# Kernel tuning notes

Measured on AMD Instinct MI355X. Metric: run time of the kernel, lower is better.

The kernel has to match this reference:

```python
import jax, jax.numpy as jnp
import numpy as np

CODEBOOK_SIZE = 2048
LATENT_DIM = 256
COMMITMENT_BETA = 0.25
B, C, T = 16, LATENT_DIM, 2048


def setup_inputs() -> dict:
    key = jax.random.key(0)
    k1, k2 = jax.random.split(key)
    x = jax.random.normal(k1, (B, C, T), dtype=jnp.float32)
    # matches nn.Embedding.weight.data.uniform_(-1/K, 1/K)
    codebook = jax.random.uniform(
        k2, (CODEBOOK_SIZE, LATENT_DIM), dtype=jnp.float32,
        minval=-1.0 / CODEBOOK_SIZE, maxval=1.0 / CODEBOOK_SIZE)
    return {"x": x, "codebook": codebook}


def reference(x, codebook):
    b, c, t = x.shape
    # (B, C, T) -> (B*T, C)
    xf = jnp.transpose(x, (0, 2, 1)).reshape(b * t, c)
    # squared Euclidean distances; argmin is invariant to the sqrt in torch.cdist(p=2)
    x_sq = jnp.sum(xf * xf, axis=1, keepdims=True)            # (BT, 1)
    e_sq = jnp.sum(codebook * codebook, axis=1)[None, :]      # (1, K)
    d2 = x_sq - 2.0 * (xf @ codebook.T) + e_sq                # (BT, K)
    idx = jnp.argmin(d2, axis=-1)                             # (BT,)
    # gather codebook vectors -> (B, C, T)
    quant = codebook[idx].reshape(b, t, c).transpose(0, 2, 1)
    commitment_loss = COMMITMENT_BETA * jnp.mean(
        (jax.lax.stop_gradient(quant) - x) ** 2)
    codebook_loss = jnp.mean((quant - jax.lax.stop_gradient(x)) ** 2)
    # straight-through estimator
    quant_out = x + jax.lax.stop_gradient(quant - x)
    return quant_out, codebook_loss, commitment_loss, idx.reshape(b, t)
```

## Files before the change

kernel.cpp:

```cpp
#include <hip/hip_runtime.h>
#include <hip/hip_bf16.h>

#define KCODES 2048
#define DIM 256
#define TLEN 2048
#define NB 16
#define NROWS (NB * TLEN)
#define NELEM (NB * DIM * TLEN)
#define LOSS_OFF NELEM
#define IDX_OFF (NELEM + 2)

#define AMARGIN 1.8e-3f

#define CCAP 48

#define OFF_XSQ   0ull
#define OFF_ESQ   131072ull
#define OFF_KEYS  139264ull
#define OFF_BSUM  401408ull
#define OFF_EHI   532480ull
#define OFF_XHI   1581056ull
#define OFF_AMAX  18358272ull
#define OFF_MASK  22552576ull
#define WS_NEED   30941184ull

typedef __bf16 bf16x8 __attribute__((ext_vector_type(8)));
typedef float  f32x4  __attribute__((ext_vector_type(4)));

__device__ __forceinline__ float sq_rn(float v) { return __fmul_rn(v, v); }

__device__ __forceinline__ unsigned encf(float f) {
    unsigned u = __float_as_uint(f);
    return (u & 0x80000000u) ? ~u : (u | 0x80000000u);
}
__device__ __forceinline__ float decf(unsigned k) {
    return __uint_as_float((k & 0x80000000u) ? (k & 0x7FFFFFFFu) : ~k);
}

__global__ __launch_bounds__(256) void xsq_kernel(const float* __restrict__ x,
                                                  float* __restrict__ xsq) {
    int m = blockIdx.x * 256 + threadIdx.x;
    int b = m >> 11, t = m & (TLEN - 1);
    const float* p = x + (size_t)b * DIM * TLEN + t;
    float h[2];
#pragma unroll
    for (int half = 0; half < 2; ++half) {
        int c0 = half * 128;
        float r[8];
#pragma unroll
        for (int j = 0; j < 8; ++j) r[j] = sq_rn(p[(size_t)(c0 + j) * TLEN]);
        for (int i = 8; i < 128; i += 8) {
#pragma unroll
            for (int j = 0; j < 8; ++j)
                r[j] = __fadd_rn(r[j], sq_rn(p[(size_t)(c0 + i + j) * TLEN]));
        }
        h[half] = __fadd_rn(__fadd_rn(__fadd_rn(r[0], r[1]), __fadd_rn(r[2], r[3])),
                            __fadd_rn(__fadd_rn(r[4], r[5]), __fadd_rn(r[6], r[7])));
    }
    xsq[m] = __fadd_rn(h[0], h[1]);
}

__global__ __launch_bounds__(256) void esq_kernel(const float* __restrict__ cb,
                                                  float* __restrict__ esq) {
    int k = blockIdx.x * 256 + threadIdx.x;
    const float* p = cb + (size_t)k * DIM;
    float h[2];
#pragma unroll
    for (int half = 0; half < 2; ++half) {
        int c0 = half * 128;
        float r[8];
#pragma unroll
        for (int j = 0; j < 8; ++j) r[j] = sq_rn(p[c0 + j]);
        for (int i = 8; i < 128; i += 8) {
#pragma unroll
            for (int j = 0; j < 8; ++j)
                r[j] = __fadd_rn(r[j], sq_rn(p[c0 + i + j]));
        }
        h[half] = __fadd_rn(__fadd_rn(__fadd_rn(r[0], r[1]), __fadd_rn(r[2], r[3])),
                            __fadd_rn(__fadd_rn(r[4], r[5]), __fadd_rn(r[6], r[7])));
    }
    esq[k] = __fadd_rn(h[0], h[1]);
}

__global__ __launch_bounds__(256) void split_x_kernel(const float* __restrict__ x,
                                                      __hip_bfloat16* __restrict__ Xhi) {
    __shared__ float tb[32][72];
    int blk = blockIdx.x;
    int tt = blk & 31, cc = (blk >> 5) & 7, b = blk >> 8;
    int c0 = cc << 5, t0 = tt << 6;
    int tid = threadIdx.x;
    {
        int c_l = tid >> 3, t8 = (tid & 7) << 3;
        const float* src = x + (size_t)b * DIM * TLEN + (size_t)(c0 + c_l) * TLEN + t0 + t8;
        float4 v0 = *reinterpret_cast<const float4*>(src);
        float4 v1 = *reinterpret_cast<const float4*>(src + 4);
        tb[c_l][t8 + 0] = v0.x; tb[c_l][t8 + 1] = v0.y; tb[c_l][t8 + 2] = v0.z; tb[c_l][t8 + 3] = v0.w;
        tb[c_l][t8 + 4] = v1.x; tb[c_l][t8 + 5] = v1.y; tb[c_l][t8 + 6] = v1.z; tb[c_l][t8 + 7] = v1.w;
    }
    __syncthreads();
    {
        int cp = tid & 3, m_l = tid >> 2;
        size_t m = (size_t)b * TLEN + t0 + m_l;
        alignas(16) __hip_bfloat16 h8[8];
#pragma unroll
        for (int j = 0; j < 8; ++j)
            h8[j] = __float2bfloat16(tb[(cp << 3) + j][m_l]);
        *reinterpret_cast<int4*>(Xhi + m * DIM + c0 + (cp << 3)) = *reinterpret_cast<int4*>(h8);
    }
}

__global__ __launch_bounds__(256) void prep_e_kernel(const float* __restrict__ cb,
                                                     __hip_bfloat16* __restrict__ Ehi,
                                                     float* __restrict__ esq) {
    int tid = threadIdx.x;
    int w = tid >> 6, lane = tid & 63;
    int k = (blockIdx.x << 2) + w;
    const float* p = cb + (size_t)k * DIM;

    float4 v = *reinterpret_cast<const float4*>(p + (lane << 2));
    alignas(8) __hip_bfloat16 h4[4];
    h4[0] = __float2bfloat16(v.x); h4[1] = __float2bfloat16(v.y);
    h4[2] = __float2bfloat16(v.z); h4[3] = __float2bfloat16(v.w);
    *reinterpret_cast<int2*>(Ehi + (size_t)k * DIM + (lane << 2)) = *reinterpret_cast<int2*>(h4);

    if (lane < 16) {
        int c0 = (lane >> 3) << 7, j = lane & 7;
        float r = sq_rn(p[c0 + j]);
        for (int i = 8; i < 128; i += 8)
            r = __fadd_rn(r, sq_rn(p[c0 + i + j]));
        float a  = __fadd_rn(r,  __shfl_xor(r, 1, 16));
        float b2 = __fadd_rn(a,  __shfl_xor(a, 2, 16));
        float h  = __fadd_rn(b2, __shfl_xor(b2, 4, 16));
        float tot = __fadd_rn(h, __shfl_xor(h, 8, 16));
        if (lane == 0) esq[k] = tot;
    }
}

__global__ __launch_bounds__(256, 4) void mfma_dist_kernel(const __hip_bfloat16* __restrict__ Xhi,
                                                           const __hip_bfloat16* __restrict__ Ehi,
                                                           unsigned* __restrict__ amax_g,
                                                           unsigned long long* __restrict__ mask_g) {
    __shared__ __hip_bfloat16 Ah[128 * 64];
    __shared__ __hip_bfloat16 Bh[128 * 64];

    int blk = blockIdx.x;
    int nt = blk & 15, mt = blk >> 4;
    int m0 = mt << 7, n0 = nt << 7;
    int tid = threadIdx.x;
    int w = tid >> 6, lane = tid & 63;
    int q = lane >> 4, c = lane & 15;
    int mhalf = w >> 1, nhalf = w & 1;

    int srow = lane >> 3;
    int scol = ((lane & 7) ^ srow) << 3;
    const __hip_bfloat16* gA = Xhi + (size_t)(m0 + (w << 5) + srow) * DIM + scol;
    const __hip_bfloat16* gB = Ehi + (size_t)(n0 + (w << 5) + srow) * DIM + scol;

    f32x4 acc[4][4];
#pragma unroll
    for (int ci = 0; ci < 4; ++ci)
#pragma unroll
        for (int mi = 0; mi < 4; ++mi) acc[ci][mi] = (f32x4){0.f, 0.f, 0.f, 0.f};

    const char* AhB = reinterpret_cast<const char*>(Ah);
    const char* BhB = reinterpret_cast<const char*>(Bh);
    int swzc = (c & 7) << 4;

    for (int kk = 0; kk < DIM; kk += 64) {
#pragma unroll
        for (int j = 0; j < 4; ++j)
            __builtin_amdgcn_global_load_lds(
                (const __attribute__((address_space(1))) unsigned int*)(gA + (size_t)(j << 3) * DIM + kk),
                (__attribute__((address_space(3))) unsigned int*)(&Ah[((w << 2) + j) << 9]),
                16, 0, 0);
#pragma unroll
        for (int j = 0; j < 4; ++j)
            __builtin_amdgcn_global_load_lds(
                (const __attribute__((address_space(1))) unsigned int*)(gB + (size_t)(j << 3) * DIM + kk),
                (__attribute__((address_space(3))) unsigned int*)(&Bh[((w << 2) + j) << 9]),
                16, 0, 0);
        __syncthreads();
#pragma unroll
        for (int kh = 0; kh < 2; ++kh) {
            int swz = ((kh << 6) | (q << 4)) ^ swzc;
            bf16x8 xf[4], cf[4];
#pragma unroll
            for (int mi = 0; mi < 4; ++mi) {
                int row = (mhalf << 6) + (mi << 4) + c;
                xf[mi] = *reinterpret_cast<const bf16x8*>(AhB + (row << 7) + swz);
            }
#pragma unroll
            for (int ci = 0; ci < 4; ++ci) {
                int row = (nhalf << 6) + (ci << 4) + c;
                cf[ci] = *reinterpret_cast<const bf16x8*>(BhB + (row << 7) + swz);
            }
#pragma unroll
            for (int ci = 0; ci < 4; ++ci)
#pragma unroll
                for (int mi = 0; mi < 4; ++mi)
                    acc[ci][mi] = __builtin_amdgcn_mfma_f32_16x16x32_bf16(cf[ci], xf[mi], acc[ci][mi], 0, 0, 0);
        }
        __syncthreads();
    }

    int tb = (nt << 1) | nhalf;
#pragma unroll
    for (int mi = 0; mi < 4; ++mi) {
        float a16[16];
#pragma unroll
        for (int ci = 0; ci < 4; ++ci)
#pragma unroll
            for (int reg = 0; reg < 4; ++reg)
                a16[ci * 4 + reg] = acc[ci][mi][reg];
        float m01 = fmaxf(fmaxf(a16[0], a16[1]), fmaxf(a16[2], a16[3]));
        float m23 = fmaxf(fmaxf(a16[4], a16[5]), fmaxf(a16[6], a16[7]));
        float m45 = fmaxf(fmaxf(a16[8], a16[9]), fmaxf(a16[10], a16[11]));
        float m67 = fmaxf(fmaxf(a16[12], a16[13]), fmaxf(a16[14], a16[15]));
        float amax = fmaxf(fmaxf(m01, m23), fmaxf(m45, m67));
        amax = fmaxf(amax, __shfl_xor(amax, 16, 64));
        amax = fmaxf(amax, __shfl_xor(amax, 32, 64));
        float thrw = amax - AMARGIN;
        unsigned long long bits = 0;
#pragma unroll
        for (int v = 0; v < 16; ++v)
            if (a16[v] >= thrw)
                bits |= 1ULL << (((v >> 2) << 4) + (q << 2) + (v & 3));
        bits |= (unsigned long long)__shfl_xor((long long)bits, 16, 64);
        bits |= (unsigned long long)__shfl_xor((long long)bits, 32, 64);
        if (q == 0) {
            int m = m0 + (mhalf << 6) + (mi << 4) + c;
            amax_g[(size_t)tb * NROWS + m] = encf(amax);
            mask_g[(size_t)tb * NROWS + m] = bits;
        }
    }
}

__global__ __launch_bounds__(256) void recheck_kernel(const float* __restrict__ x,
                                                      const float* __restrict__ cb,
                                                      const float* __restrict__ esq,
                                                      const unsigned* __restrict__ amax_g,
                                                      const unsigned long long* __restrict__ mask_g,
                                                      unsigned long long* __restrict__ keys) {
    __shared__ float xT[DIM * 33];
    __shared__ int clist[32][CCAP];
    __shared__ int ccnt[32];

    int tid = threadIdx.x;
    int blk = blockIdx.x;
    int b = blk >> 6, t0 = (blk & 63) << 5;
    const float* xb = x + (size_t)b * DIM * TLEN + t0;

    if (tid < 32) ccnt[tid] = 0;
    {
        int tl = tid & 31, c8 = tid >> 5;
        for (int cc = 0; cc < 32; ++cc) {
            int c = (cc << 3) + c8;
            xT[c * 33 + tl] = xb[(size_t)c * TLEN + tl];
        }
    }
    __syncthreads();

    int g = tid >> 3, l3 = tid & 7;
    int m = (b << 11) + t0 + g;

    float h[2];
#pragma unroll
    for (int half = 0; half < 2; ++half) {
        int c0 = half * 128;
        float r = sq_rn(xT[(c0 + l3) * 33 + g]);
        for (int i = 8; i < 128; i += 8)
            r = __fadd_rn(r, sq_rn(xT[(c0 + i + l3) * 33 + g]));
        float a = __fadd_rn(r, __shfl_xor(r, 1, 8));
        float bb = __fadd_rn(a, __shfl_xor(a, 2, 8));
        h[half] = __fadd_rn(bb, __shfl_xor(bb, 4, 8));
    }
    float xs = __fadd_rn(h[0], h[1]);

    unsigned am4[4];
    unsigned ge = 0;
#pragma unroll
    for (int j = 0; j < 4; ++j) {
        am4[j] = amax_g[(size_t)(l3 * 4 + j) * NROWS + m];
        ge = max(ge, am4[j]);
    }
    for (int off = 1; off < 8; off <<= 1)
        ge = max(ge, (unsigned)__shfl_xor((int)ge, off, 8));
    float thr = decf(ge) - AMARGIN;

#pragma unroll
    for (int j = 0; j < 4; ++j) {
        if (decf(am4[j]) >= thr) {
            unsigned long long bits = mask_g[(size_t)(l3 * 4 + j) * NROWS + m];
            while (bits) {
                int p = __ffsll((long long)bits) - 1; bits &= bits - 1;
                int pos = atomicAdd(&ccnt[g], 1);
                if (pos < CCAP) clist[g][pos] = (l3 * 4 + j) * 64 + p;
            }
        }
    }
    __syncthreads();

    int cnt = ccnt[g];
    float bd = 3.4e38f; int bi = 0x7fffffff;

    if (cnt <= CCAP) {
        for (int j = l3; j < cnt; j += 8) {
            int n = clist[g][j];
            const float* crow = cb + (size_t)n * DIM;
            float d = 0.f;
            for (int k = 0; k < DIM; k += 4) {
                float4 cv = *reinterpret_cast<const float4*>(crow + k);
                d = fmaf(xT[(k + 0) * 33 + g], cv.x, d);
                d = fmaf(xT[(k + 1) * 33 + g], cv.y, d);
                d = fmaf(xT[(k + 2) * 33 + g], cv.z, d);
                d = fmaf(xT[(k + 3) * 33 + g], cv.w, d);
            }
            float d2 = __fadd_rn(__fadd_rn(xs, -2.0f * d), esq[n]);
            if (d2 < bd || (d2 == bd && n < bi)) { bd = d2; bi = n; }
        }
    } else {
        for (int n = l3; n < KCODES; n += 8) {
            const float* crow = cb + (size_t)n * DIM;
            float d = 0.f;
            for (int k = 0; k < DIM; k += 4) {
                float4 cv = *reinterpret_cast<const float4*>(crow + k);
                d = fmaf(xT[(k + 0) * 33 + g], cv.x, d);
                d = fmaf(xT[(k + 1) * 33 + g], cv.y, d);
                d = fmaf(xT[(k + 2) * 33 + g], cv.z, d);
                d = fmaf(xT[(k + 3) * 33 + g], cv.w, d);
            }
            float d2 = __fadd_rn(__fadd_rn(xs, -2.0f * d), esq[n]);
            if (d2 < bd || (d2 == bd && n < bi)) { bd = d2; bi = n; }
        }
    }
    for (int off = 1; off < 8; off <<= 1) {
        float od = __shfl_xor(bd, off, 8);
        int   oi = __shfl_xor(bi, off, 8);
        if (od < bd || (od == bd && oi < bi)) { bd = od; bi = oi; }
    }
    if (l3 == 0)
        keys[m] = ((unsigned long long)__float_as_uint(bd) << 32) | (unsigned)(bi & 2047);
}

__global__ __launch_bounds__(256) void init_keys_kernel(unsigned long long* __restrict__ keys) {
    keys[blockIdx.x * 256 + threadIdx.x] = ~0ULL;
}

__global__ __launch_bounds__(256, 4) void dist_kernel(const float* __restrict__ x,
                                                      const float* __restrict__ cb,
                                                      const float* __restrict__ xsq,
                                                      const float* __restrict__ esq,
                                                      unsigned long long* __restrict__ keys) {
    __shared__ float As[16][128];
    __shared__ float Bs[16][132];
    int blk = blockIdx.x;
    int nt = blk & 15, mt = blk >> 4;
    int m0 = mt << 7;
    int b = m0 >> 11, t0 = m0 & (TLEN - 1);
    int n0 = nt << 7;
    int tid = threadIdx.x;
    int tm = tid >> 4, tn = tid & 15;
    const float* xbase = x + (size_t)b * DIM * TLEN + t0;
    float acc[8][8] = {};
    for (int kk = 0; kk < DIM; kk += 16) {
#pragma unroll
        for (int h = 0; h < 2; ++h) {
            int qq = tid + (h << 8);
            int k = qq >> 5, mq = (qq & 31) << 2;
            float4 v = *reinterpret_cast<const float4*>(xbase + (size_t)(kk + k) * TLEN + mq);
            *reinterpret_cast<float4*>(&As[k][mq]) = v;
        }
#pragma unroll
        for (int h = 0; h < 2; ++h) {
            int qq = tid + (h << 8);
            int nr = qq >> 2, kc = (qq & 3) << 2;
            float4 v = *reinterpret_cast<const float4*>(cb + (size_t)(n0 + nr) * DIM + kk + kc);
            Bs[kc + 0][nr] = v.x; Bs[kc + 1][nr] = v.y;
            Bs[kc + 2][nr] = v.z; Bs[kc + 3][nr] = v.w;
        }
        __syncthreads();
#pragma unroll
        for (int k = 0; k < 16; ++k) {
            float4 a0 = *reinterpret_cast<const float4*>(&As[k][tm << 2]);
            float4 a1 = *reinterpret_cast<const float4*>(&As[k][64 + (tm << 2)]);
            float4 b0 = *reinterpret_cast<const float4*>(&Bs[k][tn << 2]);
            float4 b1 = *reinterpret_cast<const float4*>(&Bs[k][64 + (tn << 2)]);
            float am[8] = {a0.x, a0.y, a0.z, a0.w, a1.x, a1.y, a1.z, a1.w};
            float bn[8] = {b0.x, b0.y, b0.z, b0.w, b1.x, b1.y, b1.z, b1.w};
#pragma unroll
            for (int mi = 0; mi < 8; ++mi)
#pragma unroll
                for (int ni = 0; ni < 8; ++ni)
                    acc[mi][ni] = fmaf(am[mi], bn[ni], acc[mi][ni]);
        }
        __syncthreads();
    }
    int cn[8]; float es[8];
#pragma unroll
    for (int ni = 0; ni < 8; ++ni) {
        cn[ni] = n0 + ((ni < 4) ? (tn << 2) + ni : 60 + (tn << 2) + ni);
        es[ni] = esq[cn[ni]];
    }
#pragma unroll
    for (int mi = 0; mi < 8; ++mi) {
        int m = m0 + ((mi < 4) ? (tm << 2) + mi : 60 + (tm << 2) + mi);
        float xs = xsq[m];
        float bd = 3.4e38f;
        int bi = 0x7fffffff;
#pragma unroll
        for (int ni = 0; ni < 8; ++ni) {
            float d2 = __fadd_rn(__fadd_rn(xs, -2.0f * acc[mi][ni]), es[ni]);
            if (d2 < bd) { bd = d2; bi = cn[ni]; }
        }
        for (int off = 1; off < 16; off <<= 1) {
            float od = __shfl_xor(bd, off, 16);
            int oi = __shfl_xor(bi, off, 16);
            if (od < bd || (od == bd && oi < bi)) { bd = od; bi = oi; }
        }
        if (tn == 0) {
            unsigned long long key =
                ((unsigned long long)__float_as_uint(bd) << 32) | (unsigned)(bi & 2047);
            atomicMin(&keys[m], key);
        }
    }
}

__global__ __launch_bounds__(256) void gather_kernel(const float* __restrict__ x,
                                                     const float* __restrict__ cb,
                                                     const unsigned long long* __restrict__ keys,
                                                     float* __restrict__ out,
                                                     float* __restrict__ bsum) {
    int tid = threadIdx.x;
    int blk = blockIdx.x;
    int c8 = blk & 31, tc = (blk >> 5) & 7, b = blk >> 8;
    int c0 = c8 << 3;
    int t = (tc << 8) + tid;
    int m = (b << 11) + t;
    unsigned idx = (unsigned)(keys[m]) & 2047u;
    const float* crow = cb + (size_t)idx * DIM + c0;
    float4 cv0 = *reinterpret_cast<const float4*>(crow);
    float4 cv1 = *reinterpret_cast<const float4*>(crow + 4);
    if (c8 == 0) out[(size_t)IDX_OFF + m] = (float)idx;

    float qv[8] = {cv0.x, cv0.y, cv0.z, cv0.w, cv1.x, cv1.y, cv1.z, cv1.w};
    __shared__ float wsum[4][8];
    int lane = tid & 63, wid = tid >> 6;
    float sv[8];
#pragma unroll
    for (int cc = 0; cc < 8; ++cc) {
        size_t e = (size_t)b * (DIM * TLEN) + (size_t)(c0 + cc) * TLEN + t;
        float xv = x[e];
        float diff = __fsub_rn(qv[cc], xv);
        out[e] = __fadd_rn(xv, diff);
        float s = __fmul_rn(diff, diff);
        for (int off = 32; off > 0; off >>= 1) s += __shfl_down(s, off, 64);
        sv[cc] = s;
    }
    if (lane == 0) {
#pragma unroll
        for (int cc = 0; cc < 8; ++cc) wsum[wid][cc] = sv[cc];
    }
    __syncthreads();
    if (tid == 0) {
#pragma unroll
        for (int cc = 0; cc < 8; ++cc)
            bsum[(b << 11) + ((c0 + cc) << 3) + tc] =
                ((wsum[0][cc] + wsum[1][cc]) + (wsum[2][cc] + wsum[3][cc]));
    }
}

__global__ __launch_bounds__(1024) void finalize_kernel(const float* __restrict__ bsum,
                                                        float* __restrict__ out) {
    double s = 0.0;
    for (int i = threadIdx.x; i < 32768; i += 1024) s += (double)bsum[i];
    for (int off = 32; off > 0; off >>= 1) s += __shfl_down(s, off, 64);
    __shared__ double wsum[16];
    int lane = threadIdx.x & 63, wid = threadIdx.x >> 6;
    if (lane == 0) wsum[wid] = s;
    __syncthreads();
    if (threadIdx.x == 0) {
        double total = 0.0;
        for (int ww = 0; ww < 16; ++ww) total += wsum[ww];
        float mean = (float)(total / (double)NELEM);
        out[LOSS_OFF] = mean;
        out[LOSS_OFF + 1] = 0.25f * mean;
    }
}

extern "C" void kernel_launch(void* const* d_in, const int* in_sizes, int n_in,
                              void* d_out, int out_size, void* d_ws, size_t ws_size,
                              hipStream_t stream) {
    const float* x  = (const float*)d_in[0];
    const float* cb = (const float*)d_in[1];
    float* out = (float*)d_out;
    char* ws = (char*)d_ws;
    float* xsq = (float*)(ws + OFF_XSQ);
    float* esq = (float*)(ws + OFF_ESQ);
    unsigned long long* keys = (unsigned long long*)(ws + OFF_KEYS);
    float* bsum = (float*)(ws + OFF_BSUM);

    if (ws_size >= WS_NEED) {
        __hip_bfloat16* Ehi = (__hip_bfloat16*)(ws + OFF_EHI);
        __hip_bfloat16* Xhi = (__hip_bfloat16*)(ws + OFF_XHI);
        unsigned* amax_g = (unsigned*)(ws + OFF_AMAX);
        unsigned long long* mask_g = (unsigned long long*)(ws + OFF_MASK);
        prep_e_kernel<<<KCODES / 4, 256, 0, stream>>>(cb, Ehi, esq);
        split_x_kernel<<<NB * 8 * 32, 256, 0, stream>>>(x, Xhi);
        mfma_dist_kernel<<<(NROWS / 128) * (KCODES / 128), 256, 0, stream>>>(
            Xhi, Ehi, amax_g, mask_g);
        recheck_kernel<<<NROWS / 32, 256, 0, stream>>>(x, cb, esq, amax_g, mask_g, keys);
    } else {
        esq_kernel<<<KCODES / 256, 256, 0, stream>>>(cb, esq);
        xsq_kernel<<<NROWS / 256, 256, 0, stream>>>(x, xsq);
        init_keys_kernel<<<NROWS / 256, 256, 0, stream>>>(keys);
        dist_kernel<<<(NROWS / 128) * (KCODES / 128), 256, 0, stream>>>(x, cb, xsq, esq, keys);
    }
    gather_kernel<<<(NB * 8 * 32), 256, 0, stream>>>(x, cb, keys, out, bsum);
    finalize_kernel<<<1, 1024, 0, stream>>>(bsum, out);
}
```

Baseline: 195.4 us.

## Fuse gather and loss into recheck, merge prep kernels, swizzle MFMA block order

Merges the codebook and x preparation kernels into a single launch. The recheck kernel now writes the indices, the straight-through output and per-block squared-difference sums directly, which removes the keys round trip and the separate gather pass over x. The MFMA distance kernel remaps block IDs so consecutive blocks spread across M tiles, likely to improve L2 reuse or XCD locality. A new double-precision finalize kernel reduces the per-block sums. This adds shared memory in recheck (a second 33KB tile), which may lower occupancy.

New measurement: 185.2 us. 1.06x faster.

```diff
diff --git a/kernel.cpp b/kernel.cpp
--- a/kernel.cpp
+++ b/kernel.cpp
@@ -82,57 +82,57 @@
     esq[k] = __fadd_rn(h[0], h[1]);
 }
 
-__global__ __launch_bounds__(256) void split_x_kernel(const float* __restrict__ x,
-                                                      __hip_bfloat16* __restrict__ Xhi) {
-    __shared__ float tb[32][72];
-    int blk = blockIdx.x;
-    int tt = blk & 31, cc = (blk >> 5) & 7, b = blk >> 8;
-    int c0 = cc << 5, t0 = tt << 6;
+__global__ __launch_bounds__(256) void prep_kernel(const float* __restrict__ cb,
+                                                   const float* __restrict__ x,
+                                                   __hip_bfloat16* __restrict__ Ehi,
+                                                   float* __restrict__ esq,
+                                                   __hip_bfloat16* __restrict__ Xhi) {
     int tid = threadIdx.x;
-    {
-        int c_l = tid >> 3, t8 = (tid & 7) << 3;
-        const float* src = x + (size_t)b * DIM * TLEN + (size_t)(c0 + c_l) * TLEN + t0 + t8;
-        float4 v0 = *reinterpret_cast<const float4*>(src);
-        float4 v1 = *reinterpret_cast<const float4*>(src + 4);
-        tb[c_l][t8 + 0] = v0.x; tb[c_l][t8 + 1] = v0.y; tb[c_l][t8 + 2] = v0.z; tb[c_l][t8 + 3] = v0.w;
-        tb[c_l][t8 + 4] = v1.x; tb[c_l][t8 + 5] = v1.y; tb[c_l][t8 + 6] = v1.z; tb[c_l][t8 + 7] = v1.w;
-    }
-    __syncthreads();
-    {
-        int cp = tid & 3, m_l = tid >> 2;
-        size_t m = (size_t)b * TLEN + t0 + m_l;
-        alignas(16) __hip_bfloat16 h8[8];
-#pragma unroll
-        for (int j = 0; j < 8; ++j)
-            h8[j] = __float2bfloat16(tb[(cp << 3) + j][m_l]);
-        *reinterpret_cast<int4*>(Xhi + m * DIM + c0 + (cp << 3)) = *reinterpret_cast<int4*>(h8);
-    }
-}
-
-__global__ __launch_bounds__(256) void prep_e_kernel(const float* __restrict__ cb,
-                                                     __hip_bfloat16* __restrict__ Ehi,
-                                                     float* __restrict__ esq) {
-    int tid = threadIdx.x;
-    int w = tid >> 6, lane = tid & 63;
-    int k = (blockIdx.x << 2) + w;
-    const float* p = cb + (size_t)k * DIM;
-
-    float4 v = *reinterpret_cast<const float4*>(p + (lane << 2));
-    alignas(8) __hip_bfloat16 h4[4];
-    h4[0] = __float2bfloat16(v.x); h4[1] = __float2bfloat16(v.y);
-    h4[2] = __float2bfloat16(v.z); h4[3] = __float2bfloat16(v.w);
-    *reinterpret_cast<int2*>(Ehi + (size_t)k * DIM + (lane << 2)) = *reinterpret_cast<int2*>(h4);
-
-    if (lane < 16) {
-        int c0 = (lane >> 3) << 7, j = lane & 7;
-        float r = sq_rn(p[c0 + j]);
-        for (int i = 8; i < 128; i += 8)
-            r = __fadd_rn(r, sq_rn(p[c0 + i + j]));
-        float a  = __fadd_rn(r,  __shfl_xor(r, 1, 16));
-        float b2 = __fadd_rn(a,  __shfl_xor(a, 2, 16));
-        float h  = __fadd_rn(b2, __shfl_xor(b2, 4, 16));
-        float tot = __fadd_rn(h, __shfl_xor(h, 8, 16));
-        if (lane == 0) esq[k] = tot;
+    if (blockIdx.x < 512) {
+        int w = tid >> 6, lane = tid & 63;
+        int k = ((int)blockIdx.x << 2) + w;
+        const float* p = cb + (size_t)k * DIM;
+
+        float4 v = *reinterpret_cast<const float4*>(p + (lane << 2));
+        alignas(8) __hip_bfloat16 h4[4];
+        h4[0] = __float2bfloat16(v.x); h4[1] = __float2bfloat16(v.y);
+        h4[2] = __float2bfloat16(v.z); h4[3] = __float2bfloat16(v.w);
+        *reinterpret_cast<int2*>(Ehi + (size_t)k * DIM + (lane << 2)) = *reinterpret_cast<int2*>(h4);
+
+        if (lane < 16) {
+            int c0 = (lane >> 3) << 7, j = lane & 7;
+            float r = sq_rn(p[c0 + j]);
+            for (int i = 8; i < 128; i += 8)
+                r = __fadd_rn(r, sq_rn(p[c0 + i + j]));
+            float a  = __fadd_rn(r,  __shfl_xor(r, 1, 16));
+            float b2 = __fadd_rn(a,  __shfl_xor(a, 2, 16));
+            float h  = __fadd_rn(b2, __shfl_xor(b2, 4, 16));
+            float tot = __fadd_rn(h, __shfl_xor(h, 8, 16));
+            if (lane == 0) esq[k] = tot;
+        }
+    } else {
+        __shared__ float tb[32][72];
+        int blk = blockIdx.x - 512;
+        int tt = blk & 31, cc = (blk >> 5) & 7, b = blk >> 8;
+        int c0 = cc << 5, t0 = tt << 6;
+        {
+            int c_l = tid >> 3, t8 = (tid & 7) << 3;
+            const float* src = x + (size_t)b * DIM * TLEN + (size_t)(c0 + c_l) * TLEN + t0 + t8;
+            float4 v0 = *reinterpret_cast<const float4*>(src);
+            float4 v1 = *reinterpret_cast<const float4*>(src + 4);
+            tb[c_l][t8 + 0] = v0.x; tb[c_l][t8 + 1] = v0.y; tb[c_l][t8 + 2] = v0.z; tb[c_l][t8 + 3] = v0.w;
+            tb[c_l][t8 + 4] = v1.x; tb[c_l][t8 + 5] = v1.y; tb[c_l][t8 + 6] = v1.z; tb[c_l][t8 + 7] = v1.w;
+        }
+        __syncthreads();
+        {
+            int cp = tid & 3, m_l = tid >> 2;
+            size_t m = (size_t)b * TLEN + t0 + m_l;
+            alignas(16) __hip_bfloat16 h8[8];
+#pragma unroll
+            for (int j = 0; j < 8; ++j)
+                h8[j] = __float2bfloat16(tb[(cp << 3) + j][m_l]);
+            *reinterpret_cast<int4*>(Xhi + m * DIM + c0 + (cp << 3)) = *reinterpret_cast<int4*>(h8);
+        }
     }
 }
 
@@ -143,7 +143,8 @@
     __shared__ __hip_bfloat16 Ah[128 * 64];
     __shared__ __hip_bfloat16 Bh[128 * 64];
 
-    int blk = blockIdx.x;
+    int blk = (int)blockIdx.x;
+    blk = (blk & 7) * 512 + (blk >> 3);
     int nt = blk & 15, mt = blk >> 4;
     int m0 = mt << 7, n0 = nt << 7;
     int tid = threadIdx.x;
@@ -235,15 +236,19 @@
     }
 }
 
-__global__ __launch_bounds__(256) void recheck_kernel(const float* __restrict__ x,
-                                                      const float* __restrict__ cb,
-                                                      const float* __restrict__ esq,
-                                                      const unsigned* __restrict__ amax_g,
-                                                      const unsigned long long* __restrict__ mask_g,
-                                                      unsigned long long* __restrict__ keys) {
+__global__ __launch_bounds__(256) void recheck_out_kernel(const float* __restrict__ x,
+                                                          const float* __restrict__ cb,
+                                                          const float* __restrict__ esq,
+                                                          const unsigned* __restrict__ amax_g,
+                                                          const unsigned long long* __restrict__ mask_g,
+                                                          float* __restrict__ out,
+                                                          double* __restrict__ bsum) {
     __shared__ float xT[DIM * 33];
+    __shared__ float qT[DIM * 33];
     __shared__ int clist[32][CCAP];
     __shared__ int ccnt[32];
+    __shared__ int bidx[32];
+    __shared__ double dsum[4];
 
     int tid = threadIdx.x;
     int blk = blockIdx.x;
@@ -338,8 +343,65 @@
         int   oi = __shfl_xor(bi, off, 8);
         if (od < bd || (od == bd && oi < bi)) { bd = od; bi = oi; }
     }
-    if (l3 == 0)
-        keys[m] = ((unsigned long long)__float_as_uint(bd) << 32) | (unsigned)(bi & 2047);
+    if (l3 == 0) {
+        int idx = bi & 2047;
+        bidx[g] = idx;
+        out[(size_t)IDX_OFF + m] = (float)idx;
+    }
+    __syncthreads();
+
+    {
+        int idx = bidx[g];
+        const float* crow = cb + (size_t)idx * DIM + (l3 << 5);
+#pragma unroll
+        for (int j = 0; j < 8; ++j) {
+            float4 v = *reinterpret_cast<const float4*>(crow + (j << 2));
+            int c = (l3 << 5) + (j << 2);
+            qT[(c + 0) * 33 + g] = v.x;
+            qT[(c + 1) * 33 + g] = v.y;
+            qT[(c + 2) * 33 + g] = v.z;
+            qT[(c + 3) * 33 + g] = v.w;
+        }
+    }
+    __syncthreads();
+
+    {
+        int tl = tid & 31, cbase = tid >> 5;
+        float* ob = out + (size_t)b * DIM * TLEN + t0;
+        double ds = 0.0;
+        for (int cc = 0; cc < 32; ++cc) {
+            int c = (cc << 3) + cbase;
+            float xv = xT[c * 33 + tl];
+            float qv = qT[c * 33 + tl];
+            float diff = __fsub_rn(qv, xv);
+            ob[(size_t)c * TLEN + tl] = __fadd_rn(xv, diff);
+            ds += (double)__fmul_rn(diff, diff);
+        }
+        for (int off = 32; off > 0; off >>= 1) ds += __shfl_down(ds, off, 64);
+        int lane = tid & 63, wid = tid >> 6;
+        if (lane == 0) dsum[wid] = ds;
+    }
+    __syncthreads();
+    if (tid == 0)
+        bsum[(size_t)blk * 8] = (dsum[0] + dsum[1]) + (dsum[2] + dsum[3]);
+}
+
+__global__ __launch_bounds__(256) void finalize_d_kernel(const double* __restrict__ bsum,
+                                                         float* __restrict__ out) {
+    __shared__ double dsum[4];
+    int tid = threadIdx.x;
+    double s2 = bsum[(size_t)tid * 8] + bsum[(size_t)(tid + 256) * 8]
+              + bsum[(size_t)(tid + 512) * 8] + bsum[(size_t)(tid + 768) * 8];
+    for (int off = 32; off > 0; off >>= 1) s2 += __shfl_down(s2, off, 64);
+    int lane = tid & 63, wid = tid >> 6;
+    if (lane == 0) dsum[wid] = s2;
+    __syncthreads();
+    if (tid == 0) {
+        double total = (dsum[0] + dsum[1]) + (dsum[2] + dsum[3]);
+        float mean = (float)(total / (double)NELEM);
+        out[LOSS_OFF] = mean;
+        out[LOSS_OFF + 1] = 0.25f * mean;
+    }
 }
 
 __global__ __launch_bounds__(256) void init_keys_kernel(unsigned long long* __restrict__ keys) {
@@ -496,25 +558,27 @@
     char* ws = (char*)d_ws;
     float* xsq = (float*)(ws + OFF_XSQ);
     float* esq = (float*)(ws + OFF_ESQ);
-    unsigned long long* keys = (unsigned long long*)(ws + OFF_KEYS);
-    float* bsum = (float*)(ws + OFF_BSUM);
 
     if (ws_size >= WS_NEED) {
         __hip_bfloat16* Ehi = (__hip_bfloat16*)(ws + OFF_EHI);
         __hip_bfloat16* Xhi = (__hip_bfloat16*)(ws + OFF_XHI);
         unsigned* amax_g = (unsigned*)(ws + OFF_AMAX);
         unsigned long long* mask_g = (unsigned long long*)(ws + OFF_MASK);
-        prep_e_kernel<<<KCODES / 4, 256, 0, stream>>>(cb, Ehi, esq);
-        split_x_kernel<<<NB * 8 * 32, 256, 0, stream>>>(x, Xhi);
+        double* bsum_d = (double*)(ws + OFF_BSUM);
+        prep_kernel<<<512 + NB * 8 * 32, 256, 0, stream>>>(cb, x, Ehi, esq, Xhi);
         mfma_dist_kernel<<<(NROWS / 128) * (KCODES / 128), 256, 0, stream>>>(
             Xhi, Ehi, amax_g, mask_g);
-        recheck_kernel<<<NROWS / 32, 256, 0, stream>>>(x, cb, esq, amax_g, mask_g, keys);
+        recheck_out_kernel<<<NROWS / 32, 256, 0, stream>>>(
+            x, cb, esq, amax_g, mask_g, out, bsum_d);
+        finalize_d_kernel<<<1, 256, 0, stream>>>(bsum_d, out);
     } else {
+        unsigned long long* keys = (unsigned long long*)(ws + OFF_KEYS);
+        float* bsum = (float*)(ws + OFF_BSUM);
         esq_kernel<<<KCODES / 256, 256, 0, stream>>>(cb, esq);
         xsq_kernel<<<NROWS / 256, 256, 0, stream>>>(x, xsq);
         init_keys_kernel<<<NROWS / 256, 256, 0, stream>>>(keys);
         dist_kernel<<<(NROWS / 128) * (KCODES / 128), 256, 0, stream>>>(x, cb, xsq, esq, keys);
-    }
-    gather_kernel<<<(NB * 8 * 32), 256, 0, stream>>>(x, cb, keys, out, bsum);
-    finalize_kernel<<<1, 1024, 0, stream>>>(bsum, out);
-}
+        gather_kernel<<<(NB * 8 * 32), 256, 0, stream>>>(x, cb, keys, out, bsum);
+        finalize_kernel<<<1, 1024, 0, stream>>>(bsum, out);
+    }
+}
```
